# Optimization experiments

Hardware: AMD Instinct MI355X
Metric: run time of the kernel (lower is better)

The kernel has to match this reference:

```python
import jax, jax.numpy as jnp
from jax import lax
import numpy as np

B, S, V, E, H, K = 128, 512, 32000, 128, 128, 32  # H = hidden_dim//2 per direction
START, END = 30, 31


def _lstm_dir(x, h0, c0, W_ih, W_hh, b):
    # x: [S, B, E]; PyTorch gate order: i, f, g, o
    def step(carry, xt):
        h, c = carry
        gates = xt @ W_ih.T + h @ W_hh.T + b  # [B, 4H]
        i, f, g, o = jnp.split(gates, 4, axis=1)
        c = jax.nn.sigmoid(f) * c + jax.nn.sigmoid(i) * jnp.tanh(g)
        h = jax.nn.sigmoid(o) * jnp.tanh(c)
        return (h, c), h
    _, hs = lax.scan(step, (h0, c0), x)
    return hs  # [S, B, H]


def _get_features(sentence, embed_table, W_ih_f, W_hh_f, b_ih_f, b_hh_f,
                  W_ih_b, W_hh_b, b_ih_b, b_hh_b, W_out, b_out, h0, c0):
    emb = embed_table[sentence]            # [B, S, E]
    x = emb.transpose(1, 0, 2)             # [S, B, E]
    hf = _lstm_dir(x, h0[0], c0[0], W_ih_f, W_hh_f, b_ih_f + b_hh_f)
    hb = _lstm_dir(x[::-1], h0[1], c0[1], W_ih_b, W_hh_b, b_ih_b + b_hh_b)[::-1]
    out = jnp.concatenate([hf, hb], axis=-1).transpose(1, 0, 2)  # [B, S, 2H]
    return out @ W_out.T + b_out           # [B, S, K]


def _numerator(feats, tags, transitions):
    b = tags.shape[0]
    start = jnp.full((b, 1), START, dtype=tags.dtype)
    ext = jnp.concatenate([start, tags], axis=1)  # [B, S+1]
    trans = transitions[ext[:, :-1], ext[:, 1:]].sum(axis=1)
    emit = jnp.take_along_axis(feats, tags[:, :, None], axis=2)[..., 0].sum(axis=1)
    return trans + emit + transitions[tags[:, -1], END]


def _denominator(feats, transitions):
    b, _, k = feats.shape
    init = jnp.full((b, k), -10000.0, feats.dtype).at[:, START].set(0.0)
    def step(alpha, feat):
        # alpha[b, prev]; transitions[next, prev] (as in the torch code)
        new = jax.nn.logsumexp(alpha[:, None, :] + transitions[None, :, :], axis=2) + feat
        return new, None
    alpha, _ = lax.scan(step, init, feats.transpose(1, 0, 2))
    return jax.nn.logsumexp(alpha + transitions[:, END][None, :], axis=1)


def setup_inputs():
    key = jax.random.key(0)
    ks = jax.random.split(key, 16)
    n = lambda k, shape, s=0.1: jax.random.normal(k, shape, jnp.float32) * s
    sentence = jax.random.randint(ks[0], (B, S), 0, V)
    tags = jax.random.randint(ks[1], (B, S), 0, START)
    transitions = n(ks[13], (K, K), 0.1)
    transitions = transitions.at[:, START].set(-10000.0).at[END, :].set(-10000.0)
    return dict(
        sentence=sentence, tags=tags,
        embed_table=n(ks[2], (V, E), 1.0),
        W_ih_f=n(ks[3], (4 * H, E)), W_hh_f=n(ks[4], (4 * H, H)),
        b_ih_f=n(ks[5], (4 * H,)), b_hh_f=n(ks[6], (4 * H,)),
        W_ih_b=n(ks[7], (4 * H, E)), W_hh_b=n(ks[8], (4 * H, H)),
        b_ih_b=n(ks[9], (4 * H,)), b_hh_b=n(ks[10], (4 * H,)),
        W_out=n(ks[11], (K, 2 * H)), b_out=n(ks[12], (K,)),
        transitions=transitions,
        h0=n(ks[14], (2, B, H)), c0=n(ks[15], (2, B, H)),
    )


def reference(sentence, tags, embed_table, W_ih_f, W_hh_f, b_ih_f, b_hh_f,
              W_ih_b, W_hh_b, b_ih_b, b_hh_b, W_out, b_out, transitions, h0, c0):
    feats = _get_features(sentence, embed_table, W_ih_f, W_hh_f, b_ih_f, b_hh_f,
                          W_ih_b, W_hh_b, b_ih_b, b_hh_b, W_out, b_out, h0, c0)
    num = _numerator(feats, tags, transitions)
    den = _denominator(feats, transitions)
    return jnp.mean(num - den)
```

## Files before the change

### kernel.cpp

```cpp
#include <hip/hip_runtime.h>

typedef unsigned int uint;
typedef unsigned short ushort;
typedef __fp16 half2_t __attribute__((ext_vector_type(2)));
typedef __fp16 half8_t __attribute__((ext_vector_type(8)));
typedef float floatx4 __attribute__((ext_vector_type(4)));

#define SEQ 512
#define BATCH 128
#define HID 128
#define NTAG 32
#define START_TAG 30
#define END_TAG 31

__device__ __forceinline__ float fdot2(uint a, uint b, float c) {
  return __builtin_amdgcn_fdot2(__builtin_bit_cast(half2_t, a),
                                __builtin_bit_cast(half2_t, b), c, false);
}
__device__ __forceinline__ uint packh2(float a, float b) {
  half2_t h = __builtin_amdgcn_cvt_pkrtz(a, b);
  return __builtin_bit_cast(uint, h);
}
__device__ __forceinline__ float frcp(float x) { return __builtin_amdgcn_rcpf(x); }
__device__ __forceinline__ float fsig(float x) { return frcp(1.f + __expf(-x)); }
__device__ __forceinline__ float ftanh(float x) { return 1.f - 2.f * frcp(1.f + __expf(2.f * x)); }
__device__ __forceinline__ float fexp2(float x) { return __builtin_amdgcn_exp2f(x); }
__device__ __forceinline__ float flog2(float x) { return __builtin_amdgcn_logf(x); }

__device__ __forceinline__ float quad_add(float x) {
  int a = __builtin_bit_cast(int, x);
  int b = __builtin_amdgcn_update_dpp(0, a, 0xB1, 0xF, 0xF, true);
  float y = x + __builtin_bit_cast(float, b);
  int c2 = __builtin_bit_cast(int, y);
  int d2 = __builtin_amdgcn_update_dpp(0, c2, 0x4E, 0xF, 0xF, true);
  return y + __builtin_bit_cast(float, d2);
}
template <int CTRL>
__device__ __forceinline__ float quad_bcast(float x) {
  int a = __builtin_bit_cast(int, x);
  int b = __builtin_amdgcn_update_dpp(0, a, CTRL, 0xF, 0xF, true);
  return __builtin_bit_cast(float, b);
}

__global__ __launch_bounds__(256) void prep_kernel(
    const float* __restrict__ Wihf, const float* __restrict__ Whhf,
    const float* __restrict__ bihf, const float* __restrict__ bhhf,
    const float* __restrict__ Wihb, const float* __restrict__ Whhb,
    const float* __restrict__ bihb, const float* __restrict__ bhhb,
    const float* __restrict__ Wout,
    uint* __restrict__ wihI, uint* __restrict__ whh,
    uint* __restrict__ woutp, float* __restrict__ biasI)
{
  int idx = blockIdx.x * 256 + threadIdx.x;
  if (idx < 65536) {
    int d = idx >> 15, rem = idx & 32767;
    int n = rem >> 6, dw = rem & 63;
    int m = n >> 2, q = n & 3;
    int g = q * 128 + m;
    const float* W = d ? Wihb : Wihf;
    wihI[idx] = packh2(W[g * 128 + 2 * dw], W[g * 128 + 2 * dw + 1]);
  }
  int i2 = idx - 65536;
  if (i2 >= 0 && i2 < 65536) {
    int d = i2 >> 15, rem = i2 & 32767;
    int g = rem >> 6, dw = rem & 63;
    const float* W = d ? Whhb : Whhf;
    whh[i2] = packh2(W[g * 128 + 2 * dw], W[g * 128 + 2 * dw + 1]);
  }
  int i3 = idx - 131072;
  if (i3 >= 0 && i3 < 4096) {
    int k = i3 >> 7, dw = i3 & 127;
    float a, b2;
    if (dw < 64) { a = Wout[k * 256 + 2 * dw]; b2 = Wout[k * 256 + 2 * dw + 1]; }
    else { int j = dw - 64; a = Wout[k * 256 + 128 + 2 * j]; b2 = Wout[k * 256 + 128 + 2 * j + 1]; }
    woutp[i3] = packh2(a, b2);
  }
  int i4 = idx - 135168;
  if (i4 >= 0 && i4 < 1024) {
    int d = i4 >> 9, n = i4 & 511;
    int g = (n & 3) * 128 + (n >> 2);
    biasI[i4] = d ? (bihb[g] + bhhb[g]) : (bihf[g] + bhhf[g]);
  }
}

__global__ __launch_bounds__(256, 2) void gemmx_kernel(
    const int* __restrict__ sentence, const float* __restrict__ embed,
    const uint* __restrict__ wihI, const float* __restrict__ biasI,
    uint* __restrict__ gatex, int chunk)
{
  int blk = blockIdx.x;
  int tl = blk & 127, nb = (blk >> 7) & 3, d = blk >> 9;
  int t = chunk * 128 + tl;
  int s = d ? (511 - t) : t;
  __shared__ int tok[128];
  int tid = threadIdx.x;
  if (tid < 128) tok[tid] = sentence[tid * SEQ + s];
  __syncthreads();

  int w = tid >> 6, lane = tid & 63;
  int q = lane >> 4, r = lane & 15;
  int wr = w >> 1, wc = w & 1;
  int r0 = wr * 64;
  int c0 = nb * 128 + wc * 64;

  floatx4 acc[4][4];
#pragma unroll
  for (int i = 0; i < 4; ++i)
#pragma unroll
    for (int j = 0; j < 4; ++j) acc[i][j] = (floatx4){0.f, 0.f, 0.f, 0.f};

  const float4* aptr[4];
#pragma unroll
  for (int i = 0; i < 4; ++i)
    aptr[i] = (const float4*)(embed + (size_t)tok[r0 + i * 16 + r] * HID) + q * 2;
  const uint4* bptr[4];
#pragma unroll
  for (int j = 0; j < 4; ++j)
    bptr[j] = (const uint4*)(wihI + ((size_t)d * 512 + c0 + j * 16 + r) * 64) + q;

#pragma unroll
  for (int kc = 0; kc < 4; ++kc) {
    half8_t af[4], bf[4];
#pragma unroll
    for (int i = 0; i < 4; ++i) {
      float4 x0 = aptr[i][kc * 8];
      float4 x1 = aptr[i][kc * 8 + 1];
      uint4 u;
      u.x = packh2(x0.x, x0.y); u.y = packh2(x0.z, x0.w);
      u.z = packh2(x1.x, x1.y); u.w = packh2(x1.z, x1.w);
      af[i] = __builtin_bit_cast(half8_t, u);
    }
#pragma unroll
    for (int j = 0; j < 4; ++j)
      bf[j] = __builtin_bit_cast(half8_t, bptr[j][kc * 4]);
#pragma unroll
    for (int i = 0; i < 4; ++i)
#pragma unroll
      for (int j = 0; j < 4; ++j)
        acc[i][j] = __builtin_amdgcn_mfma_f32_16x16x32_f16(af[i], bf[j], acc[i][j], 0, 0, 0);
  }

  __fp16* gat = ((__fp16*)gatex) + (size_t)d * 16384 * 512;
#pragma unroll
  for (int j = 0; j < 4; ++j) {
    int n = c0 + j * 16 + r;
    float bb = biasI[d * 512 + n];
#pragma unroll
    for (int i = 0; i < 4; ++i) {
      int rb = r0 + i * 16 + q * 4;
#pragma unroll
      for (int reg = 0; reg < 4; ++reg) {
        float v = acc[i][j][reg] + bb;
        gat[((size_t)(tl * 128 + rb + reg)) * 512 + n] = (__fp16)v;
      }
    }
  }
}

__global__ __attribute__((amdgpu_waves_per_eu(2, 2))) __launch_bounds__(512)
void lstm_kernel(
    const uint* __restrict__ gatex, const uint* __restrict__ whh,
    const float* __restrict__ h0, const float* __restrict__ c0,
    float* __restrict__ statec, uint* __restrict__ hh, int chunk)
{
  const float L2E = 1.4426950408889634f;
  const int wg = blockIdx.x;
  const int d = wg >> 7, b = wg & 127;
  const int tid = threadIdx.x;
  const int kq = tid & 3, m = tid >> 2;

  __shared__ __align__(16) __fp16 hist[128][128];

  const bool isg = (kq == 2);
  const float sl = isg ? (2.f * L2E) : (-L2E);
  const float Ac = isg ? -2.f : 1.f;
  const float Bc = isg ? 1.f : 0.f;

  const uint4* wh4 = (const uint4*)whh + (size_t)d * 8192;
  uint4 wreg[4][4];
#pragma unroll
  for (int g = 0; g < 4; ++g) {
    const uint4* row = wh4 + ((size_t)(g * 128 + m)) * 16 + kq * 4;
#pragma unroll
    for (int i = 0; i < 4; ++i) wreg[g][i] = row[i];
  }

  float c = (chunk == 0) ? c0[(size_t)(d * 128 + b) * 128 + m]
                         : statec[(size_t)(d * 128 + b) * 128 + m];

  if (tid < 64) {
    uint* h127 = (uint*)&hist[127][0];
    if (chunk == 0) {
      float2 hv = ((const float2*)(h0 + (size_t)(d * 128 + b) * 128))[tid];
      h127[tid] = packh2(hv.x, hv.y);
    } else {
      int sprev = d ? (511 - (chunk * 128 - 1)) : (chunk * 128 - 1);
      h127[tid] = hh[((size_t)(d * 512 + sprev) * 128 + b) * 64 + tid];
    }
  }
  const ushort* gxp = (const ushort*)gatex + (size_t)d * 8388608 +
                      (size_t)b * 512 + 4 * m + kq;

  auto step = [&](int tl_, ushort gxh) {
    float a0 = 0.f, a1 = 0.f, a2 = 0.f, a3 = 0.f;
    float b0 = 0.f, b1 = 0.f, b2 = 0.f, b3 = 0.f;
    const uint4* z4 = (const uint4*)(&hist[(tl_ + 127) & 127][kq * 32]);
#pragma unroll
    for (int i = 0; i < 2; ++i) {
      uint4 z = z4[i];
      a0 = fdot2(z.x, wreg[0][i].x, a0);
      a0 = fdot2(z.y, wreg[0][i].y, a0);
      a0 = fdot2(z.z, wreg[0][i].z, a0);
      a0 = fdot2(z.w, wreg[0][i].w, a0);
      a1 = fdot2(z.x, wreg[1][i].x, a1);
      a1 = fdot2(z.y, wreg[1][i].y, a1);
      a1 = fdot2(z.z, wreg[1][i].z, a1);
      a1 = fdot2(z.w, wreg[1][i].w, a1);
      a2 = fdot2(z.x, wreg[2][i].x, a2);
      a2 = fdot2(z.y, wreg[2][i].y, a2);
      a2 = fdot2(z.z, wreg[2][i].z, a2);
      a2 = fdot2(z.w, wreg[2][i].w, a2);
      a3 = fdot2(z.x, wreg[3][i].x, a3);
      a3 = fdot2(z.y, wreg[3][i].y, a3);
      a3 = fdot2(z.z, wreg[3][i].z, a3);
      a3 = fdot2(z.w, wreg[3][i].w, a3);
    }
#pragma unroll
    for (int i = 2; i < 4; ++i) {
      uint4 z = z4[i];
      b0 = fdot2(z.x, wreg[0][i].x, b0);
      b0 = fdot2(z.y, wreg[0][i].y, b0);
      b0 = fdot2(z.z, wreg[0][i].z, b0);
      b0 = fdot2(z.w, wreg[0][i].w, b0);
      b1 = fdot2(z.x, wreg[1][i].x, b1);
      b1 = fdot2(z.y, wreg[1][i].y, b1);
      b1 = fdot2(z.z, wreg[1][i].z, b1);
      b1 = fdot2(z.w, wreg[1][i].w, b1);
      b2 = fdot2(z.x, wreg[2][i].x, b2);
      b2 = fdot2(z.y, wreg[2][i].y, b2);
      b2 = fdot2(z.z, wreg[2][i].z, b2);
      b2 = fdot2(z.w, wreg[2][i].w, b2);
      b3 = fdot2(z.x, wreg[3][i].x, b3);
      b3 = fdot2(z.y, wreg[3][i].y, b3);
      b3 = fdot2(z.z, wreg[3][i].z, b3);
      b3 = fdot2(z.w, wreg[3][i].w, b3);
    }
    a0 += b0; a1 += b1; a2 += b2; a3 += b3;
    a0 = quad_add(a0);
    a1 = quad_add(a1);
    a2 = quad_add(a2);
    a3 = quad_add(a3);
    float s01 = (kq & 1) ? a1 : a0;
    float s23 = (kq & 1) ? a3 : a2;
    float own = (kq & 2) ? s23 : s01;
    own += (float)__builtin_bit_cast(__fp16, gxh);
    float e = fexp2(own * sl);
    float r = frcp(1.f + e);
    float out = Ac * r + Bc;
    float ig = quad_bcast<0x00>(out);
    float fg = quad_bcast<0x55>(out);
    float gg = quad_bcast<0xAA>(out);
    float og = quad_bcast<0xFF>(out);
    c = fg * c + ig * gg;
    float e2 = fexp2(c * (2.f * L2E));
    float r2 = frcp(1.f + e2);
    float th = 1.f - 2.f * r2;
    float hv = og * th;

    if (kq == 0) hist[tl_][m] = (__fp16)hv;
    __builtin_amdgcn_sched_barrier(0);
    asm volatile("s_waitcnt lgkmcnt(0)");
    __builtin_amdgcn_sched_barrier(0);
    __builtin_amdgcn_s_barrier();
  };

  ushort g0 = gxp[0];
  ushort g1 = gxp[(size_t)1 * 65536];
  ushort g2 = gxp[(size_t)2 * 65536];
  ushort g3 = gxp[(size_t)3 * 65536];
  __syncthreads();

  for (int tl = 0; tl < 128; tl += 4) {
    int i0 = tl + 4 > 127 ? 127 : tl + 4;
    int i1 = tl + 5 > 127 ? 127 : tl + 5;
    int i2 = tl + 6 > 127 ? 127 : tl + 6;
    int i3 = tl + 7 > 127 ? 127 : tl + 7;
    ushort n0 = gxp[(size_t)i0 * 65536];
    ushort n1 = gxp[(size_t)i1 * 65536];
    ushort n2 = gxp[(size_t)i2 * 65536];
    ushort n3 = gxp[(size_t)i3 * 65536];
    step(tl + 0, g0);
    step(tl + 1, g1);
    step(tl + 2, g2);
    step(tl + 3, g3);
    g0 = n0; g1 = n1; g2 = n2; g3 = n3;
  }

  if (kq == 0) statec[(size_t)(d * 128 + b) * 128 + m] = c;

  int base = chunk * 128;
  for (int i = tid; i < 2048; i += 512) {
    int sl2 = i >> 4, q4 = i & 15;
    int s = d ? (511 - (base + sl2)) : (base + sl2);
    *(uint4*)(&hh[((size_t)(d * 512 + s) * 128 + b) * 64 + q4 * 4]) =
        *(const uint4*)((const uint*)&hist[sl2][0] + q4 * 4);
  }
}

__global__ __launch_bounds__(256) void outproj_kernel(
    const uint* __restrict__ hh, const uint* __restrict__ woutp,
    const float* __restrict__ bout, float* __restrict__ feats)
{
  int tid = threadIdx.x;
  int w = tid >> 6, lane = tid & 63;
  int q = lane >> 4, c = lane & 15;
  int row0 = blockIdx.x * 64 + w * 16;

  const uint4* wp4 = (const uint4*)woutp;
  uint4 bf0[8], bf1[8];
#pragma unroll
  for (int ks = 0; ks < 8; ++ks) {
    bf0[ks] = wp4[(size_t)c * 32 + ks * 4 + q];
    bf1[ks] = wp4[(size_t)(16 + c) * 32 + ks * 4 + q];
  }

  int rr = row0 + c;
  int br = rr >> 9, sr = rr & 511;
  const uint4* af4 = (const uint4*)(hh + ((size_t)(sr * BATCH + br)) * 64);
  const uint4* ab4 = (const uint4*)(hh + ((size_t)((SEQ + sr) * BATCH + br)) * 64);

  floatx4 acc0 = (floatx4){0.f, 0.f, 0.f, 0.f};
  floatx4 acc1 = (floatx4){0.f, 0.f, 0.f, 0.f};
#pragma unroll
  for (int ks = 0; ks < 8; ++ks) {
    uint4 a = (ks < 4) ? af4[ks * 4 + q] : ab4[(ks - 4) * 4 + q];
    half8_t af = __builtin_bit_cast(half8_t, a);
    acc0 = __builtin_amdgcn_mfma_f32_16x16x32_f16(
        af, __builtin_bit_cast(half8_t, bf0[ks]), acc0, 0, 0, 0);
    acc1 = __builtin_amdgcn_mfma_f32_16x16x32_f16(
        af, __builtin_bit_cast(half8_t, bf1[ks]), acc1, 0, 0, 0);
  }

  float bb0 = bout[c], bb1 = bout[16 + c];
#pragma unroll
  for (int reg = 0; reg < 4; ++reg) {
    int orow = row0 + q * 4 + reg;
    feats[(size_t)orow * 32 + c] = acc0[reg] + bb0;
    feats[(size_t)orow * 32 + 16 + c] = acc1[reg] + bb1;
  }
}

__global__ __launch_bounds__(64) void crf_num_kernel(
    const int* __restrict__ tags, const float* __restrict__ feats,
    const float* __restrict__ trans, float* __restrict__ num)
{
  int b = blockIdx.x, l = threadIdx.x;
  const int* tb = tags + b * SEQ;
  float acc = 0.f;
  for (int s = l; s < SEQ; s += 64) {
    int tg = tb[s];
    int pv = (s == 0) ? START_TAG : tb[s - 1];
    acc += trans[pv * NTAG + tg] + feats[((size_t)b * SEQ + s) * NTAG + tg];
  }
#pragma unroll
  for (int msk = 1; msk < 64; msk <<= 1) acc += __shfl_xor(acc, msk);
  if (l == 0) num[b] = acc + trans[tb[SEQ - 1] * NTAG + END_TAG];
}

__global__ __launch_bounds__(64) void crf_seg_kernel(
    const float* __restrict__ feats, const float* __restrict__ trans,
    uint* __restrict__ segP, float* __restrict__ segL)
{
  const float L2E = 1.4426950408889634f;
  int blk = blockIdx.x;
  int b = blk >> 5, j = blk & 31;
  int tstart = 1 + 16 * j;
  int nsteps = (j == 31) ? 15 : 16;
  int lane = threadIdx.x;
  int c = lane & 15, q = lane >> 4;

  half8_t afr[2];
#pragma unroll
  for (int rt = 0; rt < 2; ++rt) {
    const float* trow = trans + (rt * 16 + c) * 32 + q * 8;
    float e[8];
#pragma unroll
    for (int i = 0; i < 8; ++i) e[i] = fexp2(trow[i] * L2E);
    uint4 u;
    u.x = packh2(e[0], e[1]); u.y = packh2(e[2], e[3]);
    u.z = packh2(e[4], e[5]); u.w = packh2(e[6], e[7]);
    afr[rt] = __builtin_bit_cast(half8_t, u);
  }
  half8_t bfr[2];
#pragma unroll
  for (int ct = 0; ct < 2; ++ct) {
    uint4 u;
    uint vals[8];
#pragma unroll
    for (int i = 0; i < 8; ++i)
      vals[i] = ((q * 8 + i) == (ct * 16 + c)) ? 0x3C00u : 0u;
    u.x = vals[0] | (vals[1] << 16);
    u.y = vals[2] | (vals[3] << 16);
    u.z = vals[4] | (vals[5] << 16);
    u.w = vals[6] | (vals[7] << 16);
    bfr[ct] = __builtin_bit_cast(half8_t, u);
  }

  __shared__ __fp16 P16[32 * 36];

  const float* fb = feats + ((size_t)b * SEQ + tstart) * NTAG;
  float Lacc = 0.f;
  float4 pre0 = *(const float4*)(fb + q * 4);
  float4 pre1 = *(const float4*)(fb + 16 + q * 4);

  for (int s = 0; s < nsteps; ++s) {
    float4 f0 = pre0, f1 = pre1;
    if (s + 1 < nsteps) {
      pre0 = *(const float4*)(fb + (s + 1) * 32 + q * 4);
      pre1 = *(const float4*)(fb + (s + 1) * 32 + 16 + q * 4);
    }
    floatx4 z4 = (floatx4){0.f, 0.f, 0.f, 0.f};
    floatx4 c00 = __builtin_amdgcn_mfma_f32_16x16x32_f16(afr[0], bfr[0], z4, 0, 0, 0);
    floatx4 c01 = __builtin_amdgcn_mfma_f32_16x16x32_f16(afr[0], bfr[1], z4, 0, 0, 0);
    floatx4 c10 = __builtin_amdgcn_mfma_f32_16x16x32_f16(afr[1], bfr[0], z4, 0, 0, 0);
    floatx4 c11 = __builtin_amdgcn_mfma_f32_16x16x32_f16(afr[1], bfr[1], z4, 0, 0, 0);
    float pf0[4], pf1[4];
    pf0[0] = fexp2(f0.x * L2E); pf0[1] = fexp2(f0.y * L2E);
    pf0[2] = fexp2(f0.z * L2E); pf0[3] = fexp2(f0.w * L2E);
    pf1[0] = fexp2(f1.x * L2E); pf1[1] = fexp2(f1.y * L2E);
    pf1[2] = fexp2(f1.z * L2E); pf1[3] = fexp2(f1.w * L2E);
    float v00[4], v01[4], v10[4], v11[4];
#pragma unroll
    for (int rg = 0; rg < 4; ++rg) {
      v00[rg] = c00[rg] * pf0[rg];
      v01[rg] = c01[rg] * pf0[rg];
      v10[rg] = c10[rg] * pf1[rg];
      v11[rg] = c11[rg] * pf1[rg];
    }
    float mx = 0.f;
#pragma unroll
    for (int rg = 0; rg < 4; ++rg)
      mx = fmaxf(mx, fmaxf(fmaxf(v00[rg], v01[rg]), fmaxf(v10[rg], v11[rg])));
    uint ub = (uint)__builtin_amdgcn_readfirstlane((int)__builtin_bit_cast(uint, mx));
    int e = (int)((ub >> 23) & 255u);
    Lacc += (float)(e - 127);
    float sc = __builtin_bit_cast(float, (uint)((254 - e) << 23));

    __syncthreads();
    {
      uint2 wv2;
      wv2.x = packh2(v00[0] * sc, v00[1] * sc);
      wv2.y = packh2(v00[2] * sc, v00[3] * sc);
      *(uint2*)(&P16[c * 36 + q * 4]) = wv2;
      wv2.x = packh2(v10[0] * sc, v10[1] * sc);
      wv2.y = packh2(v10[2] * sc, v10[3] * sc);
      *(uint2*)(&P16[c * 36 + 16 + q * 4]) = wv2;
      wv2.x = packh2(v01[0] * sc, v01[1] * sc);
      wv2.y = packh2(v01[2] * sc, v01[3] * sc);
      *(uint2*)(&P16[(16 + c) * 36 + q * 4]) = wv2;
      wv2.x = packh2(v11[0] * sc, v11[1] * sc);
      wv2.y = packh2(v11[2] * sc, v11[3] * sc);
      *(uint2*)(&P16[(16 + c) * 36 + 16 + q * 4]) = wv2;
    }
    __syncthreads();
    {
      uint2 lo0 = *(const uint2*)(&P16[c * 36 + q * 8]);
      uint2 hi0 = *(const uint2*)(&P16[c * 36 + q * 8 + 4]);
      uint4 u0; u0.x = lo0.x; u0.y = lo0.y; u0.z = hi0.x; u0.w = hi0.y;
      bfr[0] = __builtin_bit_cast(half8_t, u0);
      uint2 lo1 = *(const uint2*)(&P16[(16 + c) * 36 + q * 8]);
      uint2 hi1 = *(const uint2*)(&P16[(16 + c) * 36 + q * 8 + 4]);
      uint4 u1; u1.x = lo1.x; u1.y = lo1.y; u1.z = hi1.x; u1.w = hi1.y;
      bfr[1] = __builtin_bit_cast(half8_t, u1);
    }
  }
  __syncthreads();
  uint* gp = segP + (size_t)blk * 512;
  if (lane < 32) {
    int i = lane;
#pragma unroll
    for (int tp = 0; tp < 16; ++tp) {
      uint lo = (uint)__builtin_bit_cast(unsigned short, P16[(2 * tp) * 36 + i]);
      uint hi = (uint)__builtin_bit_cast(unsigned short, P16[(2 * tp + 1) * 36 + i]);
      gp[i * 16 + tp] = lo | (hi << 16);
    }
  }
  if (lane == 0) segL[blk] = Lacc;
}

__global__ __launch_bounds__(64) void crf_comb_kernel(
    const float* __restrict__ feats, const float* __restrict__ trans,
    const uint* __restrict__ segP, const float* __restrict__ segL,
    float* __restrict__ den)
{
  const float L2E = 1.4426950408889634f, LN2 = 0.6931471805599453f;
  int b = blockIdx.x, l = threadIdx.x;
  int i = l & 31, hp = l >> 5;
  const float* fb = feats + (size_t)b * SEQ * NTAG;

  float sT = 0.f;
  for (int p = 0; p < 32; ++p) sT += fexp2(trans[i * 32 + p] * L2E);
  float v = (1.f + sT) * fexp2(fb[i] * L2E);
  float L = -10000.f * L2E;

  float vo = __shfl_xor(v, 1);
  uint pv = (i & 1) ? packh2(vo, v) : packh2(v, vo);

  const uint* gp0 = segP + (size_t)b * 32 * 512 + i * 16 + hp * 8;
  uint4 ra = *(const uint4*)(gp0);
  uint4 rb = *(const uint4*)(gp0 + 4);

  for (int seg = 0; seg < 32; ++seg) {
    uint4 ca = ra, cb = rb;
    if (seg + 1 < 32) {
      ra = *(const uint4*)(gp0 + (seg + 1) * 512);
      rb = *(const uint4*)(gp0 + (seg + 1) * 512 + 4);
    }
    float g0 = __shfl(__builtin_bit_cast(float, pv), hp * 16 + 0);
    float g1 = __shfl(__builtin_bit_cast(float, pv), hp * 16 + 2);
    float g2 = __shfl(__builtin_bit_cast(float, pv), hp * 16 + 4);
    float g3 = __shfl(__builtin_bit_cast(float, pv), hp * 16 + 6);
    float g4 = __shfl(__builtin_bit_cast(float, pv), hp * 16 + 8);
    float g5 = __shfl(__builtin_bit_cast(float, pv), hp * 16 + 10);
    float g6 = __shfl(__builtin_bit_cast(float, pv), hp * 16 + 12);
    float g7 = __shfl(__builtin_bit_cast(float, pv), hp * 16 + 14);
    float acc = 0.f;
    acc = fdot2(__builtin_bit_cast(uint, g0), ca.x, acc);
    acc = fdot2(__builtin_bit_cast(uint, g1), ca.y, acc);
    acc = fdot2(__builtin_bit_cast(uint, g2), ca.z, acc);
    acc = fdot2(__builtin_bit_cast(uint, g3), ca.w, acc);
    acc = fdot2(__builtin_bit_cast(uint, g4), cb.x, acc);
    acc = fdot2(__builtin_bit_cast(uint, g5), cb.y, acc);
    acc = fdot2(__builtin_bit_cast(uint, g6), cb.z, acc);
    acc = fdot2(__builtin_bit_cast(uint, g7), cb.w, acc);
    float sm = acc + __shfl_xor(acc, 32);
    uint ub = (uint)__builtin_amdgcn_readfirstlane((int)__builtin_bit_cast(uint, sm));
    int e = (int)((ub >> 23) & 255u);
    L += (float)(e - 127) + segL[b * 32 + seg];
    float sc = __builtin_bit_cast(float, (uint)((254 - e) << 23));
    v = sm * sc;
    float vo2 = __shfl_xor(v, 1);
    pv = (i & 1) ? packh2(vo2, v) : packh2(v, vo2);
  }
  float wv = v * fexp2(trans[i * 32 + END_TAG] * L2E);
#pragma unroll
  for (int msk = 1; msk <= 16; msk <<= 1) wv += __shfl_xor(wv, msk);
  if (l == 0) den[b] = (L + flog2(wv)) * LN2;
}

__global__ __launch_bounds__(128) void final_kernel(
    const float* __restrict__ num, const float* __restrict__ den,
    float* __restrict__ out)
{
  int tid = threadIdx.x;
  float v = num[tid] - den[tid];
#pragma unroll
  for (int msk = 1; msk < 64; msk <<= 1) v += __shfl_xor(v, msk);
  __shared__ float tmp[2];
  if ((tid & 63) == 0) tmp[tid >> 6] = v;
  __syncthreads();
  if (tid == 0) out[0] = (tmp[0] + tmp[1]) * (1.f / 128.f);
}

extern "C" void kernel_launch(void* const* d_in, const int* in_sizes, int n_in,
                              void* d_out, int out_size, void* d_ws, size_t ws_size,
                              hipStream_t stream)
{
  const int* sentence = (const int*)d_in[0];
  const int* tags = (const int*)d_in[1];
  const float* embed = (const float*)d_in[2];
  const float* Wihf = (const float*)d_in[3];
  const float* Whhf = (const float*)d_in[4];
  const float* bihf = (const float*)d_in[5];
  const float* bhhf = (const float*)d_in[6];
  const float* Wihb = (const float*)d_in[7];
  const float* Whhb = (const float*)d_in[8];
  const float* bihb = (const float*)d_in[9];
  const float* bhhb = (const float*)d_in[10];
  const float* Wout = (const float*)d_in[11];
  const float* bout = (const float*)d_in[12];
  const float* trans = (const float*)d_in[13];
  const float* h0 = (const float*)d_in[14];
  const float* c0 = (const float*)d_in[15];
  float* out = (float*)d_out;

  char* ws = (char*)d_ws;
  uint* wihI = (uint*)(ws + 0);
  uint* whh = (uint*)(ws + 262144);
  uint* woutp = (uint*)(ws + 524288);
  float* biasI = (float*)(ws + 540672);
  float* numb = (float*)(ws + 544768);
  float* denb = (float*)(ws + 545280);
  float* statec = (float*)(ws + 545792);
  uint* hh = (uint*)(ws + 1048576);
  uint* gatex = (uint*)(ws + 34603008);
  float* feats = (float*)(ws + 34603008);
  uint* segP = (uint*)(ws + 42991616);
  float* segL = (float*)(ws + 51380224);

  hipLaunchKernelGGL(prep_kernel, dim3(532), dim3(256), 0, stream,
                     Wihf, Whhf, bihf, bhhf, Wihb, Whhb, bihb, bhhb, Wout,
                     wihI, whh, woutp, biasI);
  for (int c = 0; c < 4; ++c) {
    hipLaunchKernelGGL(gemmx_kernel, dim3(1024), dim3(256), 0, stream,
                       sentence, embed, wihI, biasI, gatex, c);
    hipLaunchKernelGGL(lstm_kernel, dim3(256), dim3(512), 0, stream,
                       gatex, whh, h0, c0, statec, hh, c);
  }
  hipLaunchKernelGGL(outproj_kernel, dim3(1024), dim3(256), 0, stream,
                     hh, woutp, bout, feats);
  hipLaunchKernelGGL(crf_num_kernel, dim3(128), dim3(64), 0, stream,
                     tags, feats, trans, numb);
  hipLaunchKernelGGL(crf_seg_kernel, dim3(4096), dim3(64), 0, stream,
                     feats, trans, segP, segL);
  hipLaunchKernelGGL(crf_comb_kernel, dim3(128), dim3(64), 0, stream,
                     feats, trans, segP, segL, denb);
  hipLaunchKernelGGL(final_kernel, dim3(1), dim3(128), 0, stream,
                     numb, denb, out);
}
```

Baseline: 547.1 us.

## Run input GEMM and LSTM over the whole sequence in single launches when workspace allows

When the workspace is large enough, this computes the input-gate GEMM for all 512 timesteps in one launch, then runs the recurrence for the full sequence in one persistent LSTM launch. That replaces four chunked GEMM/LSTM launch pairs and drops the per-chunk cell-state and hidden-state save/restore. The CRF numerator kernel is folded into the CRF combine kernel to remove one more launch. The cost is a gate buffer four times larger, and the new path depends on the workspace size reaching a threshold.

```diff
diff --git a/kernel.cpp b/kernel.cpp
--- a/kernel.cpp
+++ b/kernel.cpp
@@ -22,8 +22,6 @@
   return __builtin_bit_cast(uint, h);
 }
 __device__ __forceinline__ float frcp(float x) { return __builtin_amdgcn_rcpf(x); }
-__device__ __forceinline__ float fsig(float x) { return frcp(1.f + __expf(-x)); }
-__device__ __forceinline__ float ftanh(float x) { return 1.f - 2.f * frcp(1.f + __expf(2.f * x)); }
 __device__ __forceinline__ float fexp2(float x) { return __builtin_amdgcn_exp2f(x); }
 __device__ __forceinline__ float flog2(float x) { return __builtin_amdgcn_logf(x); }
 
@@ -83,12 +81,12 @@
   }
 }
 
-__global__ __launch_bounds__(256, 2) void gemmx_kernel(
+template <bool ALLT>
+__device__ __forceinline__ void gemmx_body(
     const int* __restrict__ sentence, const float* __restrict__ embed,
     const uint* __restrict__ wihI, const float* __restrict__ biasI,
-    uint* __restrict__ gatex, int chunk)
-{
-  int blk = blockIdx.x;
+    uint* __restrict__ gatex, int chunk, int blk)
+{
   int tl = blk & 127, nb = (blk >> 7) & 3, d = blk >> 9;
   int t = chunk * 128 + tl;
   int s = d ? (511 - t) : t;
@@ -140,7 +138,9 @@
         acc[i][j] = __builtin_amdgcn_mfma_f32_16x16x32_f16(af[i], bf[j], acc[i][j], 0, 0, 0);
   }
 
-  __fp16* gat = ((__fp16*)gatex) + (size_t)d * 16384 * 512;
+  size_t dstride = ALLT ? (size_t)65536 * 512 : (size_t)16384 * 512;
+  int rowbase = (ALLT ? t : tl) * 128;
+  __fp16* gat = ((__fp16*)gatex) + (size_t)d * dstride;
 #pragma unroll
   for (int j = 0; j < 4; ++j) {
     int n = c0 + j * 16 + r;
@@ -151,9 +151,128 @@
 #pragma unroll
       for (int reg = 0; reg < 4; ++reg) {
         float v = acc[i][j][reg] + bb;
-        gat[((size_t)(tl * 128 + rb + reg)) * 512 + n] = (__fp16)v;
+        gat[((size_t)(rowbase + rb + reg)) * 512 + n] = (__fp16)v;
       }
     }
+  }
+}
+
+__global__ __launch_bounds__(256, 2) void gemmx_kernel(
+    const int* __restrict__ sentence, const float* __restrict__ embed,
+    const uint* __restrict__ wihI, const float* __restrict__ biasI,
+    uint* __restrict__ gatex, int chunk)
+{
+  gemmx_body<false>(sentence, embed, wihI, biasI, gatex, chunk, blockIdx.x);
+}
+
+__global__ __launch_bounds__(256, 2) void gemmx_all_kernel(
+    const int* __restrict__ sentence, const float* __restrict__ embed,
+    const uint* __restrict__ wihI, const float* __restrict__ biasI,
+    uint* __restrict__ gatex)
+{
+  gemmx_body<true>(sentence, embed, wihI, biasI, gatex,
+                   blockIdx.x >> 10, blockIdx.x & 1023);
+}
+
+struct LstmCtx {
+  uint4 wreg[4][4];
+  float sl, Ac, Bc;
+  int kq, m;
+};
+
+__device__ __forceinline__ void lstm_step(
+    LstmCtx& cx, __fp16 (*hist)[128], int row_r, int row_w, ushort gxh,
+    float& c)
+{
+  const float L2E = 1.4426950408889634f;
+  float a0 = 0.f, a1 = 0.f, a2 = 0.f, a3 = 0.f;
+  float b0 = 0.f, b1 = 0.f, b2 = 0.f, b3 = 0.f;
+  const uint4* z4 = (const uint4*)(&hist[row_r][cx.kq * 32]);
+#pragma unroll
+  for (int i = 0; i < 2; ++i) {
+    uint4 z = z4[i];
+    a0 = fdot2(z.x, cx.wreg[0][i].x, a0);
+    a0 = fdot2(z.y, cx.wreg[0][i].y, a0);
+    a0 = fdot2(z.z, cx.wreg[0][i].z, a0);
+    a0 = fdot2(z.w, cx.wreg[0][i].w, a0);
+    a1 = fdot2(z.x, cx.wreg[1][i].x, a1);
+    a1 = fdot2(z.y, cx.wreg[1][i].y, a1);
+    a1 = fdot2(z.z, cx.wreg[1][i].z, a1);
+    a1 = fdot2(z.w, cx.wreg[1][i].w, a1);
+    a2 = fdot2(z.x, cx.wreg[2][i].x, a2);
+    a2 = fdot2(z.y, cx.wreg[2][i].y, a2);
+    a2 = fdot2(z.z, cx.wreg[2][i].z, a2);
+    a2 = fdot2(z.w, cx.wreg[2][i].w, a2);
+    a3 = fdot2(z.x, cx.wreg[3][i].x, a3);
+    a3 = fdot2(z.y, cx.wreg[3][i].y, a3);
+    a3 = fdot2(z.z, cx.wreg[3][i].z, a3);
+    a3 = fdot2(z.w, cx.wreg[3][i].w, a3);
+  }
+#pragma unroll
+  for (int i = 2; i < 4; ++i) {
+    uint4 z = z4[i];
+    b0 = fdot2(z.x, cx.wreg[0][i].x, b0);
+    b0 = fdot2(z.y, cx.wreg[0][i].y, b0);
+    b0 = fdot2(z.z, cx.wreg[0][i].z, b0);
+    b0 = fdot2(z.w, cx.wreg[0][i].w, b0);
+    b1 = fdot2(z.x, cx.wreg[1][i].x, b1);
+    b1 = fdot2(z.y, cx.wreg[1][i].y, b1);
+    b1 = fdot2(z.z, cx.wreg[1][i].z, b1);
+    b1 = fdot2(z.w, cx.wreg[1][i].w, b1);
+    b2 = fdot2(z.x, cx.wreg[2][i].x, b2);
+    b2 = fdot2(z.y, cx.wreg[2][i].y, b2);
+    b2 = fdot2(z.z, cx.wreg[2][i].z, b2);
+    b2 = fdot2(z.w, cx.wreg[2][i].w, b2);
+    b3 = fdot2(z.x, cx.wreg[3][i].x, b3);
+    b3 = fdot2(z.y, cx.wreg[3][i].y, b3);
+    b3 = fdot2(z.z, cx.wreg[3][i].z, b3);
+    b3 = fdot2(z.w, cx.wreg[3][i].w, b3);
+  }
+  a0 += b0; a1 += b1; a2 += b2; a3 += b3;
+  a0 = quad_add(a0);
+  a1 = quad_add(a1);
+  a2 = quad_add(a2);
+  a3 = quad_add(a3);
+  float s01 = (cx.kq & 1) ? a1 : a0;
+  float s23 = (cx.kq & 1) ? a3 : a2;
+  float own = (cx.kq & 2) ? s23 : s01;
+  own += (float)__builtin_bit_cast(__fp16, gxh);
+  float e = fexp2(own * cx.sl);
+  float r = frcp(1.f + e);
+  float out = cx.Ac * r + cx.Bc;
+  float ig = quad_bcast<0x00>(out);
+  float fg = quad_bcast<0x55>(out);
+  float gg = quad_bcast<0xAA>(out);
+  float og = quad_bcast<0xFF>(out);
+  c = fg * c + ig * gg;
+  float e2 = fexp2(c * (2.f * L2E));
+  float r2 = frcp(1.f + e2);
+  float th = 1.f - 2.f * r2;
+  float hv = og * th;
+
+  if (cx.kq == 0) hist[row_w][cx.m] = (__fp16)hv;
+  __builtin_amdgcn_sched_barrier(0);
+  asm volatile("s_waitcnt lgkmcnt(0)");
+  __builtin_amdgcn_sched_barrier(0);
+  __builtin_amdgcn_s_barrier();
+}
+
+__device__ __forceinline__ void lstm_init(LstmCtx& cx, const uint* whh,
+                                          int d, int tid)
+{
+  const float L2E = 1.4426950408889634f;
+  cx.kq = tid & 3;
+  cx.m = tid >> 2;
+  const bool isg = (cx.kq == 2);
+  cx.sl = isg ? (2.f * L2E) : (-L2E);
+  cx.Ac = isg ? -2.f : 1.f;
+  cx.Bc = isg ? 1.f : 0.f;
+  const uint4* wh4 = (const uint4*)whh + (size_t)d * 8192;
+#pragma unroll
+  for (int g = 0; g < 4; ++g) {
+    const uint4* row = wh4 + ((size_t)(g * 128 + cx.m)) * 16 + cx.kq * 4;
+#pragma unroll
+    for (int i = 0; i < 4; ++i) cx.wreg[g][i] = row[i];
   }
 }
 
@@ -163,30 +282,16 @@
     const float* __restrict__ h0, const float* __restrict__ c0,
     float* __restrict__ statec, uint* __restrict__ hh, int chunk)
 {
-  const float L2E = 1.4426950408889634f;
   const int wg = blockIdx.x;
   const int d = wg >> 7, b = wg & 127;
   const int tid = threadIdx.x;
-  const int kq = tid & 3, m = tid >> 2;
 
   __shared__ __align__(16) __fp16 hist[128][128];
-
-  const bool isg = (kq == 2);
-  const float sl = isg ? (2.f * L2E) : (-L2E);
-  const float Ac = isg ? -2.f : 1.f;
-  const float Bc = isg ? 1.f : 0.f;
-
-  const uint4* wh4 = (const uint4*)whh + (size_t)d * 8192;
-  uint4 wreg[4][4];
-#pragma unroll
-  for (int g = 0; g < 4; ++g) {
-    const uint4* row = wh4 + ((size_t)(g * 128 + m)) * 16 + kq * 4;
-#pragma unroll
-    for (int i = 0; i < 4; ++i) wreg[g][i] = row[i];
-  }
-
-  float c = (chunk == 0) ? c0[(size_t)(d * 128 + b) * 128 + m]
-                         : statec[(size_t)(d * 128 + b) * 128 + m];
+  LstmCtx cx;
+  lstm_init(cx, whh, d, tid);
+
+  float c = (chunk == 0) ? c0[(size_t)(d * 128 + b) * 128 + cx.m]
+                         : statec[(size_t)(d * 128 + b) * 128 + cx.m];
 
   if (tid < 64) {
     uint* h127 = (uint*)&hist[127][0];
@@ -199,80 +304,7 @@
     }
   }
   const ushort* gxp = (const ushort*)gatex + (size_t)d * 8388608 +
-                      (size_t)b * 512 + 4 * m + kq;
-
-  auto step = [&](int tl_, ushort gxh) {
-    float a0 = 0.f, a1 = 0.f, a2 = 0.f, a3 = 0.f;
-    float b0 = 0.f, b1 = 0.f, b2 = 0.f, b3 = 0.f;
-    const uint4* z4 = (const uint4*)(&hist[(tl_ + 127) & 127][kq * 32]);
-#pragma unroll
-    for (int i = 0; i < 2; ++i) {
-      uint4 z = z4[i];
-      a0 = fdot2(z.x, wreg[0][i].x, a0);
-      a0 = fdot2(z.y, wreg[0][i].y, a0);
-      a0 = fdot2(z.z, wreg[0][i].z, a0);
-      a0 = fdot2(z.w, wreg[0][i].w, a0);
-      a1 = fdot2(z.x, wreg[1][i].x, a1);
-      a1 = fdot2(z.y, wreg[1][i].y, a1);
-      a1 = fdot2(z.z, wreg[1][i].z, a1);
-      a1 = fdot2(z.w, wreg[1][i].w, a1);
-      a2 = fdot2(z.x, wreg[2][i].x, a2);
-      a2 = fdot2(z.y, wreg[2][i].y, a2);
-      a2 = fdot2(z.z, wreg[2][i].z, a2);
-      a2 = fdot2(z.w, wreg[2][i].w, a2);
-      a3 = fdot2(z.x, wreg[3][i].x, a3);
-      a3 = fdot2(z.y, wreg[3][i].y, a3);
-      a3 = fdot2(z.z, wreg[3][i].z, a3);
-      a3 = fdot2(z.w, wreg[3][i].w, a3);
-    }
-#pragma unroll
-    for (int i = 2; i < 4; ++i) {
-      uint4 z = z4[i];
-      b0 = fdot2(z.x, wreg[0][i].x, b0);
-      b0 = fdot2(z.y, wreg[0][i].y, b0);
-      b0 = fdot2(z.z, wreg[0][i].z, b0);
-      b0 = fdot2(z.w, wreg[0][i].w, b0);
-      b1 = fdot2(z.x, wreg[1][i].x, b1);
-      b1 = fdot2(z.y, wreg[1][i].y, b1);
-      b1 = fdot2(z.z, wreg[1][i].z, b1);
-      b1 = fdot2(z.w, wreg[1][i].w, b1);
-      b2 = fdot2(z.x, wreg[2][i].x, b2);
-      b2 = fdot2(z.y, wreg[2][i].y, b2);
-      b2 = fdot2(z.z, wreg[2][i].z, b2);
-      b2 = fdot2(z.w, wreg[2][i].w, b2);
-      b3 = fdot2(z.x, wreg[3][i].x, b3);
-      b3 = fdot2(z.y, wreg[3][i].y, b3);
-      b3 = fdot2(z.z, wreg[3][i].z, b3);
-      b3 = fdot2(z.w, wreg[3][i].w, b3);
-    }
-    a0 += b0; a1 += b1; a2 += b2; a3 += b3;
-    a0 = quad_add(a0);
-    a1 = quad_add(a1);
-    a2 = quad_add(a2);
-    a3 = quad_add(a3);
-    float s01 = (kq & 1) ? a1 : a0;
-    float s23 = (kq & 1) ? a3 : a2;
-    float own = (kq & 2) ? s23 : s01;
-    own += (float)__builtin_bit_cast(__fp16, gxh);
-    float e = fexp2(own * sl);
-    float r = frcp(1.f + e);
-    float out = Ac * r + Bc;
-    float ig = quad_bcast<0x00>(out);
-    float fg = quad_bcast<0x55>(out);
-    float gg = quad_bcast<0xAA>(out);
-    float og = quad_bcast<0xFF>(out);
-    c = fg * c + ig * gg;
-    float e2 = fexp2(c * (2.f * L2E));
-    float r2 = frcp(1.f + e2);
-    float th = 1.f - 2.f * r2;
-    float hv = og * th;
-
-    if (kq == 0) hist[tl_][m] = (__fp16)hv;
-    __builtin_amdgcn_sched_barrier(0);
-    asm volatile("s_waitcnt lgkmcnt(0)");
-    __builtin_amdgcn_sched_barrier(0);
-    __builtin_amdgcn_s_barrier();
-  };
+                      (size_t)b * 512 + 4 * cx.m + cx.kq;
 
   ushort g0 = gxp[0];
   ushort g1 = gxp[(size_t)1 * 65536];
@@ -289,14 +321,14 @@
     ushort n1 = gxp[(size_t)i1 * 65536];
     ushort n2 = gxp[(size_t)i2 * 65536];
     ushort n3 = gxp[(size_t)i3 * 65536];
-    step(tl + 0, g0);
-    step(tl + 1, g1);
-    step(tl + 2, g2);
-    step(tl + 3, g3);
+    lstm_step(cx, hist, (tl + 127) & 127, tl + 0, g0, c);
+    lstm_step(cx, hist, (tl + 0) & 127, tl + 1, g1, c);
+    lstm_step(cx, hist, (tl + 1) & 127, tl + 2, g2, c);
+    lstm_step(cx, hist, (tl + 2) & 127, tl + 3, g3, c);
     g0 = n0; g1 = n1; g2 = n2; g3 = n3;
   }
 
-  if (kq == 0) statec[(size_t)(d * 128 + b) * 128 + m] = c;
+  if (cx.kq == 0) statec[(size_t)(d * 128 + b) * 128 + cx.m] = c;
 
   int base = chunk * 128;
   for (int i = tid; i < 2048; i += 512) {
@@ -304,6 +336,64 @@
     int s = d ? (511 - (base + sl2)) : (base + sl2);
     *(uint4*)(&hh[((size_t)(d * 512 + s) * 128 + b) * 64 + q4 * 4]) =
         *(const uint4*)((const uint*)&hist[sl2][0] + q4 * 4);
+  }
+}
+
+__global__ __attribute__((amdgpu_waves_per_eu(2, 2))) __launch_bounds__(512)
+void lstm_all_kernel(
+    const uint* __restrict__ gatex, const uint* __restrict__ whh,
+    const float* __restrict__ h0, const float* __restrict__ c0,
+    uint* __restrict__ hh)
+{
+  const int wg = blockIdx.x;
+  const int d = wg >> 7, b = wg & 127;
+  const int tid = threadIdx.x;
+
+  __shared__ __align__(16) __fp16 hist[128][128];
+  LstmCtx cx;
+  lstm_init(cx, whh, d, tid);
+
+  float c = c0[(size_t)(d * 128 + b) * 128 + cx.m];
+
+  if (tid < 64) {
+    uint* h127 = (uint*)&hist[127][0];
+    float2 hv = ((const float2*)(h0 + (size_t)(d * 128 + b) * 128))[tid];
+    h127[tid] = packh2(hv.x, hv.y);
+  }
+  const ushort* gxp = (const ushort*)gatex + (size_t)d * 33554432 +
+                      (size_t)b * 512 + 4 * cx.m + cx.kq;
+
+  ushort g0 = gxp[0];
+  ushort g1 = gxp[(size_t)1 * 65536];
+  ushort g2 = gxp[(size_t)2 * 65536];
+  ushort g3 = gxp[(size_t)3 * 65536];
+  __syncthreads();
+
+  for (int tl = 0; tl < 512; tl += 4) {
+    int i0 = tl + 4 > 511 ? 511 : tl + 4;
+    int i1 = tl + 5 > 511 ? 511 : tl + 5;
+    int i2 = tl + 6 > 511 ? 511 : tl + 6;
+    int i3 = tl + 7 > 511 ? 511 : tl + 7;
+    ushort n0 = gxp[(size_t)i0 * 65536];
+    ushort n1 = gxp[(size_t)i1 * 65536];
+    ushort n2 = gxp[(size_t)i2 * 65536];
+    ushort n3 = gxp[(size_t)i3 * 65536];
+    lstm_step(cx, hist, (tl + 127) & 127, (tl + 0) & 127, g0, c);
+    lstm_step(cx, hist, (tl + 0) & 127, (tl + 1) & 127, g1, c);
+    lstm_step(cx, hist, (tl + 1) & 127, (tl + 2) & 127, g2, c);
+    lstm_step(cx, hist, (tl + 2) & 127, (tl + 3) & 127, g3, c);
+    g0 = n0; g1 = n1; g2 = n2; g3 = n3;
+
+    if (((tl + 3) & 127) == 127) {
+      int base = ((tl + 3) >> 7) * 128;
+      for (int i = tid; i < 2048; i += 512) {
+        int sl2 = i >> 4, q4 = i & 15;
+        int s = d ? (511 - (base + sl2)) : (base + sl2);
+        *(uint4*)(&hh[((size_t)(d * 512 + s) * 128 + b) * 64 + q4 * 4]) =
+            *(const uint4*)((const uint*)&hist[sl2][0] + q4 * 4);
+      }
+      __syncthreads();
+    }
   }
 }
 
@@ -348,23 +438,6 @@
     feats[(size_t)orow * 32 + c] = acc0[reg] + bb0;
     feats[(size_t)orow * 32 + 16 + c] = acc1[reg] + bb1;
   }
-}
-
-__global__ __launch_bounds__(64) void crf_num_kernel(
-    const int* __restrict__ tags, const float* __restrict__ feats,
-    const float* __restrict__ trans, float* __restrict__ num)
-{
-  int b = blockIdx.x, l = threadIdx.x;
-  const int* tb = tags + b * SEQ;
-  float acc = 0.f;
-  for (int s = l; s < SEQ; s += 64) {
-    int tg = tb[s];
-    int pv = (s == 0) ? START_TAG : tb[s - 1];
-    acc += trans[pv * NTAG + tg] + feats[((size_t)b * SEQ + s) * NTAG + tg];
-  }
-#pragma unroll
-  for (int msk = 1; msk < 64; msk <<= 1) acc += __shfl_xor(acc, msk);
-  if (l == 0) num[b] = acc + trans[tb[SEQ - 1] * NTAG + END_TAG];
 }
 
 __global__ __launch_bounds__(64) void crf_seg_kernel(
@@ -489,12 +562,27 @@
 }
 
 __global__ __launch_bounds__(64) void crf_comb_kernel(
-    const float* __restrict__ feats, const float* __restrict__ trans,
-    const uint* __restrict__ segP, const float* __restrict__ segL,
+    const int* __restrict__ tags, const float* __restrict__ feats,
+    const float* __restrict__ trans, const uint* __restrict__ segP,
+    const float* __restrict__ segL, float* __restrict__ num,
     float* __restrict__ den)
 {
   const float L2E = 1.4426950408889634f, LN2 = 0.6931471805599453f;
   int b = blockIdx.x, l = threadIdx.x;
+
+  {
+    const int* tb = tags + b * SEQ;
+    float acc = 0.f;
+    for (int s = l; s < SEQ; s += 64) {
+      int tg = tb[s];
+      int pv = (s == 0) ? START_TAG : tb[s - 1];
+      acc += trans[pv * NTAG + tg] + feats[((size_t)b * SEQ + s) * NTAG + tg];
+    }
+#pragma unroll
+    for (int msk = 1; msk < 64; msk <<= 1) acc += __shfl_xor(acc, msk);
+    if (l == 0) num[b] = acc + trans[tb[SEQ - 1] * NTAG + END_TAG];
+  }
+
   int i = l & 31, hp = l >> 5;
   const float* fb = feats + (size_t)b * SEQ * NTAG;
 
@@ -601,20 +689,28 @@
   hipLaunchKernelGGL(prep_kernel, dim3(532), dim3(256), 0, stream,
                      Wihf, Whhf, bihf, bhhf, Wihb, Whhb, bihb, bhhb, Wout,
                      wihI, whh, woutp, biasI);
-  for (int c = 0; c < 4; ++c) {
-    hipLaunchKernelGGL(gemmx_kernel, dim3(1024), dim3(256), 0, stream,
-                       sentence, embed, wihI, biasI, gatex, c);
-    hipLaunchKernelGGL(lstm_kernel, dim3(256), dim3(512), 0, stream,
-                       gatex, whh, h0, c0, statec, hh, c);
-  }
+
+  bool big = ws_size >= 168820736ull;
+  if (big) {
+    hipLaunchKernelGGL(gemmx_all_kernel, dim3(4096), dim3(256), 0, stream,
+                       sentence, embed, wihI, biasI, gatex);
+    hipLaunchKernelGGL(lstm_all_kernel, dim3(256), dim3(512), 0, stream,
+                       gatex, whh, h0, c0, hh);
+  } else {
+    for (int c = 0; c < 4; ++c) {
+      hipLaunchKernelGGL(gemmx_kernel, dim3(1024), dim3(256), 0, stream,
+                         sentence, embed, wihI, biasI, gatex, c);
+      hipLaunchKernelGGL(lstm_kernel, dim3(256), dim3(512), 0, stream,
+                         gatex, whh, h0, c0, statec, hh, c);
+    }
+  }
+
   hipLaunchKernelGGL(outproj_kernel, dim3(1024), dim3(256), 0, stream,
                      hh, woutp, bout, feats);
-  hipLaunchKernelGGL(crf_num_kernel, dim3(128), dim3(64), 0, stream,
-                     tags, feats, trans, numb);
   hipLaunchKernelGGL(crf_seg_kernel, dim3(4096), dim3(64), 0, stream,
                      feats, trans, segP, segL);
   hipLaunchKernelGGL(crf_comb_kernel, dim3(128), dim3(64), 0, stream,
-                     feats, trans, segP, segL, denb);
+                     tags, feats, trans, segP, segL, numb, denb);
   hipLaunchKernelGGL(final_kernel, dim3(1), dim3(128), 0, stream,
                      numb, denb, out);
 }
```

After: 518.4 us. -5.3%, faster.
